# Kernel optimization log

Measured on AMD Instinct MI355X. Metric: run time of the kernel, lower is better.

Reference implementation:

```python
import jax, jax.numpy as jnp
import numpy as np

B = 131072
RES_DIM = 100
N_CHAMBERS = 6
CF_ITERS = 5
CF_K = 0.02

COUPLING = np.array([
    [0.0, -0.3, 0.6, 0.4, -0.2, 0.3],
    [-0.3, 0.0, -0.5, -0.7, 0.6, 0.4],
    [0.6, -0.5, 0.0, 0.3, -0.3, 0.2],
    [0.4, -0.7, 0.3, 0.0, -0.4, 0.5],
    [-0.2, 0.6, -0.3, -0.4, 0.0, 0.3],
    [0.3, 0.4, 0.2, 0.5, 0.3, 0.0],
], dtype=np.float32)
DECAY = np.array([0.9, 0.93, 0.85, 0.97, 0.88, 0.94], dtype=np.float32)


def setup_inputs() -> dict:
    key = jax.random.key(0)
    ks = jax.random.split(key, 9)
    def lin(k, fan_in, fan_out):
        kw, kb = jax.random.split(k)
        bound = 1.0 / np.sqrt(fan_in)
        W = jax.random.uniform(kw, (N_CHAMBERS, fan_in, fan_out), jnp.float32, -bound, bound)
        b = jax.random.uniform(kb, (N_CHAMBERS, fan_out), jnp.float32, -bound, bound)
        return W, b
    W1, b1 = lin(ks[0], RES_DIM, 128)
    W2, b2 = lin(ks[1], 128, 64)
    W3, b3 = lin(ks[2], 64, 32)
    W4, b4 = lin(ks[3], 32, 1)
    W4 = W4[:, :, 0]  # (6, 32)
    b4 = b4[:, 0]     # (6,)
    res = jax.random.normal(ks[4], (B, RES_DIM), jnp.float32)
    return {
        "res": res,
        "W1": W1, "b1": b1, "W2": W2, "b2": b2,
        "W3": W3, "b3": b3, "W4": W4, "b4": b4,
        "coupling": jnp.asarray(COUPLING),
        "decay": jnp.asarray(DECAY),
    }


def reference(res, W1, b1, W2, b2, W3, b3, W4, b4, coupling, decay):
    # 6 per-chamber MLP towers, batched over the chamber axis c.
    h = jax.nn.silu(jnp.einsum('bd,cdh->cbh', res, W1) + b1[:, None, :])   # (6,B,128)
    h = jax.nn.silu(jnp.einsum('cbh,cho->cbo', h, W2) + b2[:, None, :])    # (6,B,64)
    h = jax.nn.silu(jnp.einsum('cbh,cho->cbo', h, W3) + b3[:, None, :])    # (6,B,32)
    raw = (jnp.einsum('cbh,ch->cb', h, W4) + b4[:, None]).T                # (B,6)
    # 5-step coupled sigmoid recurrence on the tiny (B,6) state.
    act = jax.nn.sigmoid(raw)
    for _ in range(CF_ITERS):
        delta = ((act * decay) @ coupling) * CF_K
        act = jax.nn.sigmoid(raw + delta)
    return act, raw
```

## Files before the change

### kernel.cpp

```cpp
#include <hip/hip_runtime.h>
#include <hip/hip_bf16.h>
#include <stdint.h>

#define B_TOTAL 131072

typedef __attribute__((ext_vector_type(8))) short short8;
typedef __attribute__((ext_vector_type(16))) float float16v;

#define CH_U16 24576
#define oF2 14336
#define oF3 22528
#define BF16_TOT (6 * CH_U16)
#define F32_BASE (BF16_TOT / 2)
#define sB1 0
#define sB2 768
#define sB3 1152
#define sW4 1344
#define sB4 1536
#define sCP 1542
#define sDC 1578
#define NSMALL 1584
#define CONV_TOT (BF16_TOT + NSMALL)

#define sWF3 14336
#define BUF_U16 16384

#define GLB_AS __attribute__((address_space(1)))
#define LDS_AS __attribute__((address_space(3)))

__device__ __forceinline__ float bf16_as_f32(uint16_t u) {
    union { uint32_t i; float f; } v; v.i = ((uint32_t)u) << 16; return v.f;
}
__device__ __forceinline__ uint16_t f2bf(float f) {
    uint32_t u = __float_as_uint(f);
    return (uint16_t)((u + 0x7FFFu + ((u >> 16) & 1u)) >> 16);
}
__device__ __forceinline__ float sigmoidf_fast(float x) {
    return __builtin_amdgcn_rcpf(1.0f + __expf(-x));
}
__device__ __forceinline__ float siluf(float x) { return x * sigmoidf_fast(x); }

__device__ __forceinline__ float readsrc(const void* p, int off, bool bf) {
    return bf ? bf16_as_f32(((const uint16_t*)p)[off]) : ((const float*)p)[off];
}

__device__ __forceinline__ uint32_t cvtpk_bf16(float lo, float hi) {
    uint32_t r;
    asm("v_cvt_pk_bf16_f32 %0, %1, %2" : "=v"(r) : "v"(lo), "v"(hi));
    return r;
}
__device__ __forceinline__ uint32_t silu2bf(float a, float b) {
    return cvtpk_bf16(siluf(a), siluf(b));
}
__device__ __forceinline__ void plane32swap(uint32_t& a, uint32_t& b) {
    asm("v_permlane32_swap_b32 %0, %1" : "+v"(a), "+v"(b));
}

__global__ void convert_kernel(const void* W1, const void* b1, const void* W2, const void* b2,
                               const void* W3, const void* b3, const void* W4, const void* b4,
                               const void* cp, const void* dc, uint16_t* __restrict__ wsb) {
    const bool bf = (((const uint32_t*)cp)[0] != 0u);
    int idx = blockIdx.x * 256 + threadIdx.x;
    if (idx >= CONV_TOT) return;
    if (idx < BF16_TOT) {
        int c = idx / CH_U16;
        int r = idx - c * CH_U16;
        float v;
        if (r < oF2) {
            int f = r >> 9, rem = r & 511, l = rem >> 3, e = rem & 7;
            int ct = f / 7, kb = f - ct * 7;
            int n = ct * 32 + (l & 31), k = kb * 16 + (l >> 5) * 8 + e;
            v = (k < 100) ? readsrc(W1, c * 12800 + k * 128 + n, bf) : 0.0f;
        } else if (r < oF3) {
            int j = r - oF2;
            int f = j >> 9, rem = j & 511, l = rem >> 3, e = rem & 7;
            int ct2 = f >> 3, kb = f & 7;
            int n = ct2 * 32 + (l & 31), k = kb * 16 + (l >> 5) * 8 + e;
            v = readsrc(W2, c * 8192 + k * 64 + n, bf);
        } else {
            int j = r - oF3;
            int kb = j >> 9, rem = j & 511, l = rem >> 3, e = rem & 7;
            int n = (l & 31), k = kb * 16 + (l >> 5) * 8 + e;
            v = readsrc(W3, c * 2048 + k * 32 + n, bf);
        }
        wsb[idx] = f2bf(v);
    } else {
        int fi = idx - BF16_TOT;
        float v;
        if      (fi < sB2)  v = readsrc(b1, fi, bf);
        else if (fi < sB3)  v = readsrc(b2, fi - sB2, bf);
        else if (fi < sW4)  v = readsrc(b3, fi - sB3, bf);
        else if (fi < sB4)  v = readsrc(W4, fi - sW4, bf);
        else if (fi < sCP)  v = readsrc(b4, fi - sB4, bf);
        else if (fi < sDC)  v = readsrc(cp, fi - sCP, bf);
        else                v = readsrc(dc, fi - sDC, bf);
        ((float*)wsb)[F32_BASE + fi] = v;
    }
}

union Frag { uint4 u4; uint2 u2[2]; uint32_t u[4]; short8 s8; uint16_t h[8]; };

__global__ __launch_bounds__(512, 4)
void chambers_mfma(const void* __restrict__ resv, const uint16_t* __restrict__ wsb,
                   const uint32_t* __restrict__ cpw, float* __restrict__ outF) {
    const float* wsf = (const float*)wsb;
    const bool bfin = (cpw[0] != 0u);
    const int tid = threadIdx.x;
    const int w = tid >> 6, l = tid & 63;
    const int l5 = l & 31, q2 = l >> 5;
    const int row = blockIdx.x * 256 + w * 32 + l5;

    __shared__ __align__(16) uint16_t sW[2 * BUF_U16];
    __shared__ __align__(16) float sB[NSMALL];

#define STAGE(CC)                                                              \
    {                                                                          \
        const uint16_t* gsrc = wsb + (CC) * CH_U16;                            \
        uint16_t* ldst = sW + ((CC) & 1) * BUF_U16;                            \
        _Pragma("unroll")                                                      \
        for (int r = 0; r < 4; ++r) {                                          \
            const int i = r * 8 + w;                                           \
            const int gi = (i < 28) ? i : (i + 16);                            \
            __builtin_amdgcn_global_load_lds(                                  \
                (const GLB_AS uint32_t*)(gsrc + gi * 512 + l * 8),             \
                (LDS_AS uint32_t*)(ldst + i * 512), 16, 0, 0);                 \
        }                                                                      \
    }

    STAGE(0)

    for (int i = tid; i < NSMALL; i += 512) sB[i] = wsf[F32_BASE + i];

    Frag R[7];
    if (bfin) {
        const uint16_t* bp = (const uint16_t*)resv + (size_t)row * 100;
#pragma unroll
        for (int kb = 0; kb < 6; ++kb) {
            const int k0 = kb * 16 + q2 * 8;
            R[kb].u2[0] = *(const uint2*)(bp + k0);
            R[kb].u2[1] = *(const uint2*)(bp + k0 + 4);
        }
        R[6].u4 = make_uint4(0, 0, 0, 0);
        if (q2 == 0) R[6].u2[0] = *(const uint2*)(bp + 96);
    } else {
        const float* fp = (const float*)resv + (size_t)row * 100;
#pragma unroll
        for (int kb = 0; kb < 6; ++kb) {
            const int k0 = kb * 16 + q2 * 8;
            float4 x0 = *(const float4*)(fp + k0);
            float4 x1 = *(const float4*)(fp + k0 + 4);
            R[kb].u[0] = cvtpk_bf16(x0.x, x0.y);
            R[kb].u[1] = cvtpk_bf16(x0.z, x0.w);
            R[kb].u[2] = cvtpk_bf16(x1.x, x1.y);
            R[kb].u[3] = cvtpk_bf16(x1.z, x1.w);
        }
        R[6].u4 = make_uint4(0, 0, 0, 0);
        if (q2 == 0) {
            float4 x0 = *(const float4*)(fp + 96);
            R[6].u[0] = cvtpk_bf16(x0.x, x0.y);
            R[6].u[1] = cvtpk_bf16(x0.z, x0.w);
        }
    }

    __syncthreads();

    float raw0 = 0.f, raw1 = 0.f, raw2 = 0.f, raw3 = 0.f, raw4 = 0.f, raw5 = 0.f;
    uint32_t pk1[16][2];
    uint32_t pk2[8][2];

#pragma unroll 1
    for (int c = 0; c < 6; ++c) {
        const uint16_t* const bufc = sW + (c & 1) * BUF_U16;
        if (c < 5) STAGE(c + 1)

#pragma unroll
        for (int ct = 0; ct < 4; ++ct) {
            float16v acc;
#pragma unroll
            for (int ar = 0; ar < 4; ++ar) {
                const float4 bv = *(const float4*)(sB + sB1 + c * 128 + ct * 32 + ar * 8 + q2 * 4);
                acc[4 * ar + 0] = bv.x; acc[4 * ar + 1] = bv.y;
                acc[4 * ar + 2] = bv.z; acc[4 * ar + 3] = bv.w;
            }
#pragma unroll
            for (int kb = 0; kb < 7; ++kb) {
                Frag Af; Af.u4 = *(const uint4*)(bufc + ((ct * 7 + kb) * 64 + l) * 8);
                acc = __builtin_amdgcn_mfma_f32_32x32x16_bf16(Af.s8, R[kb].s8, acc, 0, 0, 0);
            }
#pragma unroll
            for (int ar = 0; ar < 4; ++ar) {
                pk1[ct * 4 + ar][0] = silu2bf(acc[4 * ar + 0], acc[4 * ar + 1]);
                pk1[ct * 4 + ar][1] = silu2bf(acc[4 * ar + 2], acc[4 * ar + 3]);
            }
        }

        const uint16_t* gF2 = wsb + c * CH_U16 + oF2;
#pragma unroll
        for (int ct2 = 0; ct2 < 2; ++ct2) {
            float16v acc;
#pragma unroll
            for (int ar = 0; ar < 4; ++ar) {
                const float4 bv = *(const float4*)(sB + sB2 + c * 64 + ct2 * 32 + ar * 8 + q2 * 4);
                acc[4 * ar + 0] = bv.x; acc[4 * ar + 1] = bv.y;
                acc[4 * ar + 2] = bv.z; acc[4 * ar + 3] = bv.w;
            }
#pragma unroll
            for (int kb = 0; kb < 8; ++kb) {
                uint32_t x0 = pk1[2 * kb][0], y0 = pk1[2 * kb + 1][0];
                uint32_t x1 = pk1[2 * kb][1], y1 = pk1[2 * kb + 1][1];
                plane32swap(x0, y0);
                plane32swap(x1, y1);
                Frag Hf; Hf.u[0] = x0; Hf.u[1] = x1; Hf.u[2] = y0; Hf.u[3] = y1;
                Frag Af; Af.u4 = *(const uint4*)(gF2 + ((ct2 * 8 + kb) * 64 + l) * 8);
                acc = __builtin_amdgcn_mfma_f32_32x32x16_bf16(Af.s8, Hf.s8, acc, 0, 0, 0);
            }
#pragma unroll
            for (int ar = 0; ar < 4; ++ar) {
                pk2[ct2 * 4 + ar][0] = silu2bf(acc[4 * ar + 0], acc[4 * ar + 1]);
                pk2[ct2 * 4 + ar][1] = silu2bf(acc[4 * ar + 2], acc[4 * ar + 3]);
            }
        }

        {
            float16v acc;
#pragma unroll
            for (int ar = 0; ar < 4; ++ar) {
                const float4 bv = *(const float4*)(sB + sB3 + c * 32 + ar * 8 + q2 * 4);
                acc[4 * ar + 0] = bv.x; acc[4 * ar + 1] = bv.y;
                acc[4 * ar + 2] = bv.z; acc[4 * ar + 3] = bv.w;
            }
#pragma unroll
            for (int kb = 0; kb < 4; ++kb) {
                uint32_t x0 = pk2[2 * kb][0], y0 = pk2[2 * kb + 1][0];
                uint32_t x1 = pk2[2 * kb][1], y1 = pk2[2 * kb + 1][1];
                plane32swap(x0, y0);
                plane32swap(x1, y1);
                Frag Hf; Hf.u[0] = x0; Hf.u[1] = x1; Hf.u[2] = y0; Hf.u[3] = y1;
                Frag Af; Af.u4 = *(const uint4*)(bufc + sWF3 + (kb * 64 + l) * 8);
                acc = __builtin_amdgcn_mfma_f32_32x32x16_bf16(Af.s8, Hf.s8, acc, 0, 0, 0);
            }
            float part = 0.f;
#pragma unroll
            for (int ar = 0; ar < 4; ++ar) {
                const float4 wv = *(const float4*)(sB + sW4 + c * 32 + ar * 8 + q2 * 4);
                part = fmaf(siluf(acc[4 * ar + 0]), wv.x, part);
                part = fmaf(siluf(acc[4 * ar + 1]), wv.y, part);
                part = fmaf(siluf(acc[4 * ar + 2]), wv.z, part);
                part = fmaf(siluf(acc[4 * ar + 3]), wv.w, part);
            }
            part += __shfl_xor(part, 32);
            const float rv = part + sB[sB4 + c];
            raw0 = (c == 0) ? rv : raw0;
            raw1 = (c == 1) ? rv : raw1;
            raw2 = (c == 2) ? rv : raw2;
            raw3 = (c == 3) ? rv : raw3;
            raw4 = (c == 4) ? rv : raw4;
            raw5 = (c == 5) ? rv : raw5;
        }

        if (c < 5) __syncthreads();
    }

    const float rv6[6] = {raw0, raw1, raw2, raw3, raw4, raw5};
    float av[6];
#pragma unroll
    for (int c = 0; c < 6; ++c) av[c] = sigmoidf_fast(rv6[c]);
    const float K = 0.02f;
#pragma unroll 1
    for (int it = 0; it < 5; ++it) {
        float tt[6];
#pragma unroll
        for (int i = 0; i < 6; ++i) tt[i] = av[i] * sB[sDC + i] * K;
#pragma unroll
        for (int j = 0; j < 6; ++j) {
            float dl = 0.0f;
#pragma unroll
            for (int i = 0; i < 6; ++i) dl = fmaf(tt[i], sB[sCP + i * 6 + j], dl);
            av[j] = sigmoidf_fast(rv6[j] + dl);
        }
    }
    if (q2 == 0) {
        float2* oa = (float2*)(outF + (size_t)row * 6);
        oa[0] = make_float2(av[0], av[1]);
        oa[1] = make_float2(av[2], av[3]);
        oa[2] = make_float2(av[4], av[5]);
        float2* orw = (float2*)(outF + (size_t)B_TOTAL * 6 + (size_t)row * 6);
        orw[0] = make_float2(rv6[0], rv6[1]);
        orw[1] = make_float2(rv6[2], rv6[3]);
        orw[2] = make_float2(rv6[4], rv6[5]);
    }
#undef STAGE
}

extern "C" void kernel_launch(void* const* d_in, const int* in_sizes, int n_in,
                              void* d_out, int out_size, void* d_ws, size_t ws_size,
                              hipStream_t stream) {
    uint16_t* wsb = (uint16_t*)d_ws;
    convert_kernel<<<(CONV_TOT + 255) / 256, 256, 0, stream>>>(
        d_in[1], d_in[2], d_in[3], d_in[4], d_in[5], d_in[6], d_in[7], d_in[8],
        d_in[9], d_in[10], wsb);
    chambers_mfma<<<B_TOTAL / 256, 512, 0, stream>>>(
        d_in[0], wsb, (const uint32_t*)d_in[9], (float*)d_out);
}
```

Measured before the change: 165.9 us.

## Permute W2/W3 K layout to drop permlane swaps and stage all weights in LDS

The convert kernel now permutes the K index of W2 and W3 so the packed layer activations can be fed straight into the next MFMA as B operands. This removes the v_permlane32_swap shuffles between layers. The kernel also stages the whole chamber's weights, including W2 (previously read from global), in a single LDS buffer. That replaces the double-buffered prefetch with a blocking load between two barriers each chamber. The cost is that weight loads no longer overlap compute, and LDS use grows per block, which may reduce occupancy.

```diff
diff --git a/kernel.cpp b/kernel.cpp
--- a/kernel.cpp
+++ b/kernel.cpp
@@ -22,9 +22,6 @@
 #define NSMALL 1584
 #define CONV_TOT (BF16_TOT + NSMALL)
 
-#define sWF3 14336
-#define BUF_U16 16384
-
 #define GLB_AS __attribute__((address_space(1)))
 #define LDS_AS __attribute__((address_space(3)))
 
@@ -51,9 +48,6 @@
 }
 __device__ __forceinline__ uint32_t silu2bf(float a, float b) {
     return cvtpk_bf16(siluf(a), siluf(b));
-}
-__device__ __forceinline__ void plane32swap(uint32_t& a, uint32_t& b) {
-    asm("v_permlane32_swap_b32 %0, %1" : "+v"(a), "+v"(b));
 }
 
 __global__ void convert_kernel(const void* W1, const void* b1, const void* W2, const void* b2,
@@ -75,12 +69,14 @@
             int j = r - oF2;
             int f = j >> 9, rem = j & 511, l = rem >> 3, e = rem & 7;
             int ct2 = f >> 3, kb = f & 7;
-            int n = ct2 * 32 + (l & 31), k = kb * 16 + (l >> 5) * 8 + e;
+            int n = ct2 * 32 + (l & 31);
+            int k = 32 * (kb >> 1) + 8 * (e >> 1) + 4 * (l >> 5) + 2 * (kb & 1) + (e & 1);
             v = readsrc(W2, c * 8192 + k * 64 + n, bf);
         } else {
             int j = r - oF3;
             int kb = j >> 9, rem = j & 511, l = rem >> 3, e = rem & 7;
-            int n = (l & 31), k = kb * 16 + (l >> 5) * 8 + e;
+            int n = (l & 31);
+            int k = 32 * (kb >> 1) + 8 * (e >> 1) + 4 * (l >> 5) + 2 * (kb & 1) + (e & 1);
             v = readsrc(W3, c * 2048 + k * 32 + n, bf);
         }
         wsb[idx] = f2bf(v);
@@ -100,6 +96,8 @@
 
 union Frag { uint4 u4; uint2 u2[2]; uint32_t u[4]; short8 s8; uint16_t h[8]; };
 
+#define Z16 {0.f,0.f,0.f,0.f,0.f,0.f,0.f,0.f,0.f,0.f,0.f,0.f,0.f,0.f,0.f,0.f}
+
 __global__ __launch_bounds__(512, 4)
 void chambers_mfma(const void* __restrict__ resv, const uint16_t* __restrict__ wsb,
                    const uint32_t* __restrict__ cpw, float* __restrict__ outF) {
@@ -110,25 +108,22 @@
     const int l5 = l & 31, q2 = l >> 5;
     const int row = blockIdx.x * 256 + w * 32 + l5;
 
-    __shared__ __align__(16) uint16_t sW[2 * BUF_U16];
+    __shared__ __align__(16) uint16_t sW[CH_U16];
     __shared__ __align__(16) float sB[NSMALL];
 
 #define STAGE(CC)                                                              \
     {                                                                          \
         const uint16_t* gsrc = wsb + (CC) * CH_U16;                            \
-        uint16_t* ldst = sW + ((CC) & 1) * BUF_U16;                            \
         _Pragma("unroll")                                                      \
-        for (int r = 0; r < 4; ++r) {                                          \
-            const int i = r * 8 + w;                                           \
-            const int gi = (i < 28) ? i : (i + 16);                            \
+        for (int rr = 0; rr < 6; ++rr) {                                       \
+            const int i = rr * 8 + w;                   \
             __builtin_amdgcn_global_load_lds(                                  \
-                (const GLB_AS uint32_t*)(gsrc + gi * 512 + l * 8),             \
-                (LDS_AS uint32_t*)(ldst + i * 512), 16, 0, 0);                 \
+                (const GLB_AS uint32_t*)(gsrc + i * 512 + l * 8),              \
+                (LDS_AS uint32_t*)(sW + i * 512), 16, 0, 0);                   \
         }                                                                      \
     }
 
     STAGE(0)
-
     for (int i = tid; i < NSMALL; i += 512) sB[i] = wsf[F32_BASE + i];
 
     Frag R[7];
@@ -165,14 +160,11 @@
     __syncthreads();
 
     float raw0 = 0.f, raw1 = 0.f, raw2 = 0.f, raw3 = 0.f, raw4 = 0.f, raw5 = 0.f;
-    uint32_t pk1[16][2];
-    uint32_t pk2[8][2];
+    Frag pk1f[2][4];
+    Frag pk2f[2][2];
 
 #pragma unroll 1
     for (int c = 0; c < 6; ++c) {
-        const uint16_t* const bufc = sW + (c & 1) * BUF_U16;
-        if (c < 5) STAGE(c + 1)
-
 #pragma unroll
         for (int ct = 0; ct < 4; ++ct) {
             float16v acc;
@@ -182,19 +174,19 @@
                 acc[4 * ar + 0] = bv.x; acc[4 * ar + 1] = bv.y;
                 acc[4 * ar + 2] = bv.z; acc[4 * ar + 3] = bv.w;
             }
+            const uint16_t* fp1 = sW + (ct * 7) * 512 + l * 8;
 #pragma unroll
             for (int kb = 0; kb < 7; ++kb) {
-                Frag Af; Af.u4 = *(const uint4*)(bufc + ((ct * 7 + kb) * 64 + l) * 8);
+                Frag Af; Af.u4 = *(const uint4*)(fp1 + kb * 512);
                 acc = __builtin_amdgcn_mfma_f32_32x32x16_bf16(Af.s8, R[kb].s8, acc, 0, 0, 0);
             }
 #pragma unroll
             for (int ar = 0; ar < 4; ++ar) {
-                pk1[ct * 4 + ar][0] = silu2bf(acc[4 * ar + 0], acc[4 * ar + 1]);
-                pk1[ct * 4 + ar][1] = silu2bf(acc[4 * ar + 2], acc[4 * ar + 3]);
-            }
-        }
-
-        const uint16_t* gF2 = wsb + c * CH_U16 + oF2;
+                pk1f[0][ct].u[ar] = silu2bf(acc[4 * ar + 0], acc[4 * ar + 1]);
+                pk1f[1][ct].u[ar] = silu2bf(acc[4 * ar + 2], acc[4 * ar + 3]);
+            }
+        }
+
 #pragma unroll
         for (int ct2 = 0; ct2 < 2; ++ct2) {
             float16v acc;
@@ -204,20 +196,16 @@
                 acc[4 * ar + 0] = bv.x; acc[4 * ar + 1] = bv.y;
                 acc[4 * ar + 2] = bv.z; acc[4 * ar + 3] = bv.w;
             }
+            const uint16_t* fp2 = sW + oF2 + (ct2 * 8) * 512 + l * 8;
 #pragma unroll
             for (int kb = 0; kb < 8; ++kb) {
-                uint32_t x0 = pk1[2 * kb][0], y0 = pk1[2 * kb + 1][0];
-                uint32_t x1 = pk1[2 * kb][1], y1 = pk1[2 * kb + 1][1];
-                plane32swap(x0, y0);
-                plane32swap(x1, y1);
-                Frag Hf; Hf.u[0] = x0; Hf.u[1] = x1; Hf.u[2] = y0; Hf.u[3] = y1;
-                Frag Af; Af.u4 = *(const uint4*)(gF2 + ((ct2 * 8 + kb) * 64 + l) * 8);
-                acc = __builtin_amdgcn_mfma_f32_32x32x16_bf16(Af.s8, Hf.s8, acc, 0, 0, 0);
-            }
-#pragma unroll
-            for (int ar = 0; ar < 4; ++ar) {
-                pk2[ct2 * 4 + ar][0] = silu2bf(acc[4 * ar + 0], acc[4 * ar + 1]);
-                pk2[ct2 * 4 + ar][1] = silu2bf(acc[4 * ar + 2], acc[4 * ar + 3]);
+                Frag Af; Af.u4 = *(const uint4*)(fp2 + kb * 512);
+                acc = __builtin_amdgcn_mfma_f32_32x32x16_bf16(Af.s8, pk1f[kb & 1][kb >> 1].s8, acc, 0, 0, 0);
+            }
+#pragma unroll
+            for (int ar = 0; ar < 4; ++ar) {
+                pk2f[0][ct2].u[ar] = silu2bf(acc[4 * ar + 0], acc[4 * ar + 1]);
+                pk2f[1][ct2].u[ar] = silu2bf(acc[4 * ar + 2], acc[4 * ar + 3]);
             }
         }
 
@@ -229,15 +217,11 @@
                 acc[4 * ar + 0] = bv.x; acc[4 * ar + 1] = bv.y;
                 acc[4 * ar + 2] = bv.z; acc[4 * ar + 3] = bv.w;
             }
+            const uint16_t* fp3 = sW + oF3 + l * 8;
 #pragma unroll
             for (int kb = 0; kb < 4; ++kb) {
-                uint32_t x0 = pk2[2 * kb][0], y0 = pk2[2 * kb + 1][0];
-                uint32_t x1 = pk2[2 * kb][1], y1 = pk2[2 * kb + 1][1];
-                plane32swap(x0, y0);
-                plane32swap(x1, y1);
-                Frag Hf; Hf.u[0] = x0; Hf.u[1] = x1; Hf.u[2] = y0; Hf.u[3] = y1;
-                Frag Af; Af.u4 = *(const uint4*)(bufc + sWF3 + (kb * 64 + l) * 8);
-                acc = __builtin_amdgcn_mfma_f32_32x32x16_bf16(Af.s8, Hf.s8, acc, 0, 0, 0);
+                Frag Af; Af.u4 = *(const uint4*)(fp3 + kb * 512);
+                acc = __builtin_amdgcn_mfma_f32_32x32x16_bf16(Af.s8, pk2f[kb & 1][kb >> 1].s8, acc, 0, 0, 0);
             }
             float part = 0.f;
 #pragma unroll
@@ -258,7 +242,11 @@
             raw5 = (c == 5) ? rv : raw5;
         }
 
-        if (c < 5) __syncthreads();
+        if (c < 5) {
+            __syncthreads();
+            STAGE(c + 1)
+            __syncthreads();
+        }
     }
 
     const float rv6[6] = {raw0, raw1, raw2, raw3, raw4, raw5};
```

After: 164.5 us. Within noise of the previous version (-0.9%).
